# Performance work log

Measured on AMD Instinct MI355X. Metric: run time of the kernel, lower is better.

The kernel has to match this reference:

```python
import jax, jax.numpy as jnp
import numpy as np


def _rev_excl_cumsum(x):
    # sum over j > i along leading axis: reverse inclusive cumsum minus self
    return jnp.flip(jnp.cumsum(jnp.flip(x, 0), 0), 0) - x


def setup_inputs() -> dict:
    key = jax.random.key(0)
    k1, k2, k3, k4, k5 = jax.random.split(key, 5)
    T1, B, M = 4095, 64, 128  # t-1 existing stack entries, batch, embed dim
    V = jax.random.normal(k1, (T1, B, M), dtype=jnp.float32)
    s = jax.random.uniform(k2, (T1, B, 1), dtype=jnp.float32)
    d = jax.random.uniform(k3, (B, 1), dtype=jnp.float32)
    u = jax.random.uniform(k4, (B, 1), dtype=jnp.float32)
    v = jax.random.normal(k5, (B, M), dtype=jnp.float32)
    return {"V": V, "s": s, "d": d, "u": u, "v": v}


def reference(V, s, d, u, v):
    # V: [t-1, B, M], s: [t-1, B, 1], d,u: [B,1], v: [B,M]
    # Push v onto the stack
    Vn = jnp.concatenate([V, v[None]], axis=0)            # [t, B, M]
    # New strengths: sn[i] = relu(s[i] - relu(u - sum_{j>i} s[j])), sn[t-1] = d
    totprev = _rev_excl_cumsum(s)                          # [t-1, B, 1]
    sn_head = jax.nn.relu(s - jax.nn.relu(u[None] - totprev))
    sn = jnp.concatenate([sn_head, d[None]], axis=0)       # [t, B, 1]
    # Readout: r = sum_i min(sn[i], relu(1 - sum_{j>i} sn[j])) * Vn[i]
    tots = _rev_excl_cumsum(sn)                            # [t, B, 1]
    coeff = jnp.minimum(sn, jax.nn.relu(1.0 - tots))       # [t, B, 1]
    r = jnp.sum(coeff * Vn, axis=0)                        # [B, M]
    return Vn, sn, r
```

## Files before the change

kernel.cpp:

```cpp
#include <hip/hip_runtime.h>
#include <hip/hip_bf16.h>

#define T1 4095
#define TT 4096
#define B  64
#define M  128
#define BM (B * M)
#define ROW4 (BM / 4)
#define SCAN_THREADS 1024
#define NWAVE (SCAN_THREADS / 64)
#define EPT (TT / SCAN_THREADS)
#define IPB 32
#define HPB (IPB / 2)
#define NCHUNK (TT / IPB)

typedef float f32x4 __attribute__((ext_vector_type(4)));

__global__ __launch_bounds__(SCAN_THREADS) void scan_kernel(
    const float* __restrict__ s,
    const float* __restrict__ d,
    const float* __restrict__ u,
    float* __restrict__ sn_out,
    float* __restrict__ coeffT)
{
    const int b = blockIdx.x;
    const int t = threadIdx.x;
    const int lane = t & 63;
    const int wave = t >> 6;
    __shared__ float wtot1[NWAVE];
    __shared__ float wtot2[NWAVE];

    const int base = t * EPT;
    float sv[EPT];
    float sum = 0.f;
#pragma unroll
    for (int k = 0; k < EPT; ++k) {
        int i = base + k;
        float val = (i < T1) ? s[(size_t)i * B + b] : 0.f;
        sv[k] = val;
        sum += val;
    }

    float x = sum;
#pragma unroll
    for (int off = 1; off < 64; off <<= 1) {
        float y = __shfl_down(x, off);
        if (lane + off < 64) x += y;
    }
    if (lane == 0) wtot1[wave] = x;
    __syncthreads();
    float after = 0.f;
#pragma unroll
    for (int w = 0; w < NWAVE; ++w)
        if (w > wave) after += wtot1[w];
    float suffix = after + x - sum;

    const float ub = u[b];
    float tot = suffix;
    float snv[EPT];
#pragma unroll
    for (int k = EPT - 1; k >= 0; --k) {
        float sval = sv[k];
        snv[k] = fmaxf(sval - fmaxf(ub - tot, 0.f), 0.f);
        tot += sval;
    }
    if (t == SCAN_THREADS - 1) snv[EPT - 1] = d[b];

    float sum2 = 0.f;
#pragma unroll
    for (int k = 0; k < EPT; ++k) sum2 += snv[k];
    float x2 = sum2;
#pragma unroll
    for (int off = 1; off < 64; off <<= 1) {
        float y = __shfl_down(x2, off);
        if (lane + off < 64) x2 += y;
    }
    if (lane == 0) wtot2[wave] = x2;
    __syncthreads();
    float after2 = 0.f;
#pragma unroll
    for (int w = 0; w < NWAVE; ++w)
        if (w > wave) after2 += wtot2[w];
    float suffix2 = after2 + x2 - sum2;

    float tot2 = suffix2;
    float cv[EPT];
#pragma unroll
    for (int k = EPT - 1; k >= 0; --k) {
        float snval = snv[k];
        cv[k] = fminf(snval, fmaxf(1.f - tot2, 0.f));
        tot2 += snval;
        sn_out[(size_t)(base + k) * B + b] = snval;
    }
    f32x4 cc = { cv[0], cv[1], cv[2], cv[3] };
    *(f32x4*)(coeffT + (size_t)b * TT + base) = cc;
}

__global__ __launch_bounds__(512) void fuse_kernel(
    const float* __restrict__ V,
    const float* __restrict__ v,
    const float* __restrict__ coeffT,
    float* __restrict__ Vn,
    float* __restrict__ partials)
{
    const int bmTile = blockIdx.x;
    const int chunk  = blockIdx.y;
    const int tid  = threadIdx.x;
    const int half = tid >> 8;
    const int t    = tid & 255;
    const int bm4  = bmTile * 256 + t;
    const int b    = bm4 >> 5;
    const int i0   = chunk * IPB + half * HPB;

    float c[HPB];
    const f32x4* cp = (const f32x4*)(coeffT + (size_t)b * TT + i0);
#pragma unroll
    for (int q = 0; q < HPB / 4; ++q) {
        f32x4 cc = cp[q];
        c[4*q+0] = cc.x; c[4*q+1] = cc.y; c[4*q+2] = cc.z; c[4*q+3] = cc.w;
    }

    f32x4 acc = {0.f, 0.f, 0.f, 0.f};
    const f32x4* Vp  = (const f32x4*)V;
    f32x4*       Vnp = (f32x4*)Vn;

    const bool lastHalf = (chunk == NCHUNK - 1) && (half == 1);
    if (!lastHalf) {
#pragma unroll
        for (int k = 0; k < HPB; ++k) {
            const size_t idx = (size_t)(i0 + k) * ROW4 + bm4;
            f32x4 val = Vp[idx];
            __builtin_nontemporal_store(val, &Vnp[idx]);
            acc += c[k] * val;
        }
    } else {
#pragma unroll
        for (int k = 0; k < HPB - 1; ++k) {
            const size_t idx = (size_t)(i0 + k) * ROW4 + bm4;
            f32x4 val = Vp[idx];
            __builtin_nontemporal_store(val, &Vnp[idx]);
            acc += c[k] * val;
        }
        f32x4 val = ((const f32x4*)v)[bm4];
        __builtin_nontemporal_store(val, &Vnp[(size_t)T1 * ROW4 + bm4]);
        acc += c[HPB - 1] * val;
    }

    __shared__ f32x4 sh[256];
    if (half == 1) sh[t] = acc;
    __syncthreads();
    if (half == 0)
        ((f32x4*)partials)[(size_t)chunk * ROW4 + bm4] = acc + sh[t];
}

__global__ __launch_bounds__(256) void reduce_kernel(
    const float* __restrict__ partials,
    float* __restrict__ r)
{
    const int blk = blockIdx.x;
    const int tid = threadIdx.x;
    const int grp = tid >> 5;
    const int lane = tid & 31;
    const int out4 = blk * 32 + lane;

    f32x4 acc = {0.f, 0.f, 0.f, 0.f};
#pragma unroll 8
    for (int c = grp; c < NCHUNK; c += 8)
        acc += ((const f32x4*)partials)[(size_t)c * ROW4 + out4];

    __shared__ f32x4 sh[256];
    sh[tid] = acc;
    __syncthreads();
    if (tid < 128) sh[tid] += sh[tid + 128];
    __syncthreads();
    if (tid < 64) sh[tid] += sh[tid + 64];
    __syncthreads();
    if (tid < 32) {
        f32x4 res = sh[tid] + sh[tid + 32];
        ((f32x4*)r)[out4] = res;
    }
}

extern "C" void kernel_launch(void* const* d_in, const int* in_sizes, int n_in,
                              void* d_out, int out_size, void* d_ws, size_t ws_size,
                              hipStream_t stream) {
    const float* V = (const float*)d_in[0];
    const float* s = (const float*)d_in[1];
    const float* d = (const float*)d_in[2];
    const float* u = (const float*)d_in[3];
    const float* v = (const float*)d_in[4];

    float* out = (float*)d_out;
    float* Vn = out;
    float* sn = out + (size_t)TT * BM;
    float* r  = sn + (size_t)TT * B;

    float* coeffT   = (float*)d_ws;
    float* partials = coeffT + (size_t)B * TT;

    scan_kernel<<<B, SCAN_THREADS, 0, stream>>>(s, d, u, sn, coeffT);
    fuse_kernel<<<dim3(8, NCHUNK), 512, 0, stream>>>(V, v, coeffT, Vn, partials);
    reduce_kernel<<<64, 256, 0, stream>>>(partials, r);
}
```

Before: 59.54 us.

## Write sn transposed from scan, transpose to output via extra fuse-kernel blocks

```diff
diff --git a/kernel.cpp b/kernel.cpp
--- a/kernel.cpp
+++ b/kernel.cpp
@@ -20,15 +20,14 @@
     const float* __restrict__ s,
     const float* __restrict__ d,
     const float* __restrict__ u,
-    float* __restrict__ sn_out,
+    float* __restrict__ snT,
     float* __restrict__ coeffT)
 {
     const int b = blockIdx.x;
     const int t = threadIdx.x;
     const int lane = t & 63;
     const int wave = t >> 6;
-    __shared__ float wtot1[NWAVE];
-    __shared__ float wtot2[NWAVE];
+    __shared__ float wtot1[NWAVE], wtot2[NWAVE];
 
     const int base = t * EPT;
     float sv[EPT];
@@ -40,7 +39,6 @@
         sv[k] = val;
         sum += val;
     }
-
     float x = sum;
 #pragma unroll
     for (int off = 1; off < 64; off <<= 1) {
@@ -90,22 +88,56 @@
         float snval = snv[k];
         cv[k] = fminf(snval, fmaxf(1.f - tot2, 0.f));
         tot2 += snval;
-        sn_out[(size_t)(base + k) * B + b] = snval;
-    }
-    f32x4 cc = { cv[0], cv[1], cv[2], cv[3] };
-    *(f32x4*)(coeffT + (size_t)b * TT + base) = cc;
+    }
+    *(f32x4*)(snT + (size_t)b * TT + base) = (f32x4){snv[0], snv[1], snv[2], snv[3]};
+    *(f32x4*)(coeffT + (size_t)b * TT + base) = (f32x4){cv[0], cv[1], cv[2], cv[3]};
 }
 
 __global__ __launch_bounds__(512) void fuse_kernel(
     const float* __restrict__ V,
     const float* __restrict__ v,
     const float* __restrict__ coeffT,
+    const float* __restrict__ snT,
     float* __restrict__ Vn,
+    float* __restrict__ sn_out,
     float* __restrict__ partials)
 {
     const int bmTile = blockIdx.x;
     const int chunk  = blockIdx.y;
     const int tid  = threadIdx.x;
+
+    __shared__ __align__(16) float smem[64 * 65];
+
+    if (chunk == NCHUNK) {
+        float (*tile)[65] = (float(*)[65])smem;
+#pragma unroll 1
+        for (int j = 0; j < 8; ++j) {
+            const int g = bmTile * 8 + j;
+            {
+                const int b    = tid >> 3;
+                const int ioff = (tid & 7) * 8;
+                const f32x4* src4 = (const f32x4*)(snT + (size_t)b * TT + g * 64 + ioff);
+                f32x4 v0 = src4[0], v1 = src4[1];
+                tile[ioff+0][b] = v0.x; tile[ioff+1][b] = v0.y;
+                tile[ioff+2][b] = v0.z; tile[ioff+3][b] = v0.w;
+                tile[ioff+4][b] = v1.x; tile[ioff+5][b] = v1.y;
+                tile[ioff+6][b] = v1.z; tile[ioff+7][b] = v1.w;
+            }
+            __syncthreads();
+            {
+                const int i    = tid >> 3;
+                const int boff = (tid & 7) * 8;
+                float* dst = sn_out + (size_t)(g * 64 + i) * B + boff;
+                *(f32x4*)dst = (f32x4){tile[i][boff+0], tile[i][boff+1],
+                                       tile[i][boff+2], tile[i][boff+3]};
+                *(f32x4*)(dst + 4) = (f32x4){tile[i][boff+4], tile[i][boff+5],
+                                             tile[i][boff+6], tile[i][boff+7]};
+            }
+            __syncthreads();
+        }
+        return;
+    }
+
     const int half = tid >> 8;
     const int t    = tid & 255;
     const int bm4  = bmTile * 256 + t;
@@ -146,14 +178,14 @@
         acc += c[HPB - 1] * val;
     }
 
-    __shared__ f32x4 sh[256];
-    if (half == 1) sh[t] = acc;
+    f32x4* shc = (f32x4*)smem;
+    if (half == 1) shc[t] = acc;
     __syncthreads();
     if (half == 0)
-        ((f32x4*)partials)[(size_t)chunk * ROW4 + bm4] = acc + sh[t];
-}
-
-__global__ __launch_bounds__(256) void reduce_kernel(
+        ((f32x4*)partials)[(size_t)chunk * ROW4 + bm4] = acc + shc[t];
+}
+
+__global__ __launch_bounds__(256) void finish_kernel(
     const float* __restrict__ partials,
     float* __restrict__ r)
 {
@@ -175,10 +207,7 @@
     __syncthreads();
     if (tid < 64) sh[tid] += sh[tid + 64];
     __syncthreads();
-    if (tid < 32) {
-        f32x4 res = sh[tid] + sh[tid + 32];
-        ((f32x4*)r)[out4] = res;
-    }
+    if (tid < 32) ((f32x4*)r)[out4] = sh[tid] + sh[tid + 32];
 }
 
 extern "C" void kernel_launch(void* const* d_in, const int* in_sizes, int n_in,
@@ -196,9 +225,11 @@
     float* r  = sn + (size_t)TT * B;
 
     float* coeffT   = (float*)d_ws;
-    float* partials = coeffT + (size_t)B * TT;
-
-    scan_kernel<<<B, SCAN_THREADS, 0, stream>>>(s, d, u, sn, coeffT);
-    fuse_kernel<<<dim3(8, NCHUNK), 512, 0, stream>>>(V, v, coeffT, Vn, partials);
-    reduce_kernel<<<64, 256, 0, stream>>>(partials, r);
-}
+    float* snT      = coeffT + (size_t)B * TT;
+    float* partials = snT + (size_t)B * TT;
+
+    scan_kernel<<<B, SCAN_THREADS, 0, stream>>>(s, d, u, snT, coeffT);
+    fuse_kernel<<<dim3(8, NCHUNK + 1), 512, 0, stream>>>(V, v, coeffT, snT,
+                                                         Vn, sn, partials);
+    finish_kernel<<<64, 256, 0, stream>>>(partials, r);
+}
```

Result: no change. 60.43 us (+1.5%).
